# Performance work log

Measured on AMD Instinct MI355X. Metric: run time of the kernel, lower is better.

Reference implementation:

```python
import jax, jax.numpy as jnp
import numpy as np

N_FILTERS = 40
FILTER_SIZE = 401   # int(16000*25/1000), forced odd
POOL_STRIDE = 160   # int(16000*10/1000)
EPS = 1e-6
S_SMOOTH = 0.04     # fixed PCEN smoothing coefficient s
DELTA = 2.0         # fixed PCEN bias delta
R_MIN, R_MAX = 0.2, 1.0
HIDDEN = 32


def setup_inputs() -> dict:
    key = jax.random.key(0)
    ks = jax.random.split(key, 6)
    B, L = 8, 160000
    x = jax.random.normal(ks[0], (B, L), dtype=jnp.float32)
    # mel-initialized Gabor params (as in mel_filter_params)
    sr, fmin, fmax = 16000.0, 60.0, 7800.0
    min_mel = 1127.0 * np.log1p(fmin / 700.0)
    max_mel = 1127.0 * np.log1p(fmax / 700.0)
    peaks_mel = np.linspace(min_mel, max_mel, N_FILTERS + 2)
    peaks_hz = 700.0 * np.expm1(peaks_mel / 1127.0)
    center_freqs = jnp.asarray(peaks_hz[1:-1] * 2.0 * np.pi / sr, dtype=jnp.float32)
    z = np.sqrt(2.0 * np.log(2.0)) / np.pi
    bandwidths = jnp.asarray(z * sr / (peaks_hz[2:] - peaks_hz[:-2]), dtype=jnp.float32)
    pooling_widths = jnp.full((N_FILTERS,), 0.4, dtype=jnp.float32)
    # GRU (input_size=1, hidden=32) + head Linear(32,32)->ReLU->Linear(32,2)
    def gl(k, shape):
        return jax.random.normal(k, shape, dtype=jnp.float32) * 0.1
    w_ih = gl(ks[1], (3 * HIDDEN, 1))
    w_hh = gl(ks[2], (3 * HIDDEN, HIDDEN))
    b_ih = jnp.zeros((3 * HIDDEN,), jnp.float32)
    b_hh = jnp.zeros((3 * HIDDEN,), jnp.float32)
    hw1 = gl(ks[3], (32, HIDDEN)); hb1 = jnp.zeros((32,), jnp.float32)
    hw2 = gl(ks[4], (2, 32)); hb2 = jnp.zeros((2,), jnp.float32)
    return dict(x=x, center_freqs=center_freqs, bandwidths=bandwidths,
                pooling_widths=pooling_widths, w_ih=w_ih, w_hh=w_hh,
                b_ih=b_ih, b_hh=b_hh, hw1=hw1, hb1=hb1, hw2=hw2, hb2=hb2)


def _gabor_filterbank(x, center_freqs, bandwidths, pooling_widths):
    z = np.sqrt(2.0 * np.log(2.0)) / np.pi
    cf = jnp.clip(center_freqs, 0.0, np.pi)
    bw = jnp.clip(bandwidths, 4.0 * z, FILTER_SIZE * z)
    t = jnp.arange(-(FILTER_SIZE // 2), (FILTER_SIZE + 1) // 2, dtype=jnp.float32)
    denom = 1.0 / (jnp.sqrt(2.0 * np.pi) * bw)                        # [F]
    gauss = jnp.exp(-(t[None, :] ** 2) / (2.0 * bw[:, None] ** 2))    # [F,K]
    phase = cf[:, None] * t[None, :]                                  # [F,K]
    fr = denom[:, None] * gauss * jnp.cos(phase)
    fi = denom[:, None] * gauss * jnp.sin(phase)
    filt = jnp.concatenate([fr, fi], axis=0)[:, None, :]              # [2F,1,K]
    pad = FILTER_SIZE // 2
    y = jax.lax.conv_general_dilated(x[:, None, :], filt, (1,), [(pad, pad)])
    y = y ** 2
    y = y[:, :N_FILTERS] + y[:, N_FILTERS:]                           # squared modulus [B,F,L]
    pw = jnp.clip(pooling_widths, 2.0 / FILTER_SIZE, 0.5)
    tt = jnp.arange(FILTER_SIZE, dtype=jnp.float32) / (FILTER_SIZE - 1) - 0.5
    win = jnp.exp(-0.5 * (tt[None, :] / pw[:, None]) ** 2)[:, None, :]  # [F,1,K]
    y = jax.lax.conv_general_dilated(y, win, (POOL_STRIDE,), [(pad, pad)],
                                     feature_group_count=N_FILTERS)
    return y  # [B,F,T]


def _gru_cell(h, xin, w_ih, w_hh, b_ih, b_hh):
    gi = xin @ w_ih.T + b_ih   # [N,3H]
    gh = h @ w_hh.T + b_hh
    i_r, i_z, i_n = jnp.split(gi, 3, axis=-1)
    h_r, h_z, h_n = jnp.split(gh, 3, axis=-1)
    r = jax.nn.sigmoid(i_r + h_r)
    zz = jax.nn.sigmoid(i_z + h_z)
    n = jnp.tanh(i_n + r * h_n)
    return (1.0 - zz) * n + zz * h


def _adaptive_pcen(frames, w_ih, w_hh, b_ih, b_hh, hw1, hb1, hw2, hb2):
    B, F, T = frames.shape
    Xt = jnp.transpose(frames, (2, 0, 1))  # [T,B,F]

    def controller(x_prev, x_t):  # each [B,F] -> per-bin (alpha, r)
        xp = x_prev.reshape(-1, 1)
        xc = x_t.reshape(-1, 1)
        h = jnp.zeros((B * F, HIDDEN), frames.dtype)
        h = _gru_cell(h, xp, w_ih, w_hh, b_ih, b_hh)
        h = _gru_cell(h, xc, w_ih, w_hh, b_ih, b_hh)
        hid = jax.nn.relu(h @ hw1.T + hb1)
        logits = hid @ hw2.T + hb2  # [B*F,2]
        alpha = jax.nn.sigmoid(logits[:, 0]).reshape(B, F)
        r = (R_MIN + (R_MAX - R_MIN) * jax.nn.sigmoid(logits[:, 1])).reshape(B, F)
        return alpha, r

    def step(carry, X_t):
        M_prev, X_prev = carry
        alpha, r = controller(X_prev, X_t)
        M_t = (1.0 - S_SMOOTH) * M_prev + S_SMOOTH * X_t
        out = (X_t / (M_t + EPS) ** alpha + DELTA) ** r - DELTA ** r
        return (M_t, X_t), out

    init = (jnp.zeros((B, F), frames.dtype), Xt[0])
    _, outs = jax.lax.scan(step, init, Xt)
    return jnp.transpose(outs, (1, 2, 0))  # [B,F,T]


def reference(x, center_freqs, bandwidths, pooling_widths,
              w_ih, w_hh, b_ih, b_hh, hw1, hb1, hw2, hb2):
    frames = _gabor_filterbank(x, center_freqs, bandwidths, pooling_widths)
    return _adaptive_pcen(frames, w_ih, w_hh, b_ih, b_hh, hw1, hb1, hw2, hb2)
```

## Files before the change

### kernel.cpp

```cpp
#include <hip/hip_runtime.h>
#include <math.h>

#define NF 40
#define FS 401
#define AST 424
#define PSTRIDE 160
#define BB 8
#define LL 160000
#define PADL 256
#define LST 161024
#define TOUT 1000
#define NTILE 512
#define NCHUNKC 313
#define ROWCH 121
#define ROWST (ROWCH*8)
#define EROW 520
#define WROW 402
#define NCONVB 5032
#define TAUC 125
#define ECH (TAUC*PSTRIDE + 408)

typedef __attribute__((ext_vector_type(8))) _Float16 half8v;
typedef __attribute__((ext_vector_type(4))) _Float16 half4v;
typedef __attribute__((ext_vector_type(2))) _Float16 half2v;
typedef __attribute__((ext_vector_type(4))) float float4v;
typedef _Float16 f16;

__device__ __forceinline__ float sigm(float x) { return 1.0f / (1.0f + __expf(-x)); }
__device__ __forceinline__ float tanh_fast(float x) { return 1.0f - 2.0f / (__expf(2.0f * x) + 1.0f); }

__global__ __launch_bounds__(256) void prep_all(
    const float* __restrict__ x, const float* __restrict__ cf_,
    const float* __restrict__ bw_, const float* __restrict__ pw_,
    f16* __restrict__ xb, f16* __restrict__ Ag, float* __restrict__ winG)
{
    int blk = blockIdx.x;
    if (blk < NCONVB) {
        int i = blk * 256 + threadIdx.x;
        int b = i / LST, o = i % LST;
        float v = 0.0f;
        if (o >= PADL && o < PADL + LL) v = x[b * LL + (o - PADL)];
        xb[i] = (f16)v;
        return;
    }
    const float PI_F = 3.14159265358979323846f;
    if (blk < NCONVB + 80) {
        int row = blk - NCONVB;
        int f = row >> 1, comp = row & 1;
        float Z = sqrtf(2.0f * logf(2.0f)) / PI_F;
        float cf = fminf(fmaxf(cf_[f], 0.0f), PI_F);
        float bw = fminf(fmaxf(bw_[f], 4.0f * Z), 401.0f * Z);
        float denom = 1.0f / (sqrtf(2.0f * PI_F) * bw);
        float inv2 = 1.0f / (2.0f * bw * bw);
        for (int k = threadIdx.x; k < AST; k += 256) {
            float v = 0.0f;
            if (k < FS) {
                float t = (float)(k - 200);
                float g = denom * expf(-(t * t) * inv2);
                float sv, cv;
                sincosf(cf * t, &sv, &cv);
                v = comp ? g * sv : g * cv;
            }
            Ag[row * AST + k] = (f16)v;
        }
        return;
    }
    int f = blk - NCONVB - 80;
    float pw = fminf(fmaxf(pw_[f], 2.0f / 401.0f), 0.5f);
    float invpw = 1.0f / pw;
    for (int j = threadIdx.x; j < WROW; j += 256) {
        float w = 0.0f;
        if (j < FS) {
            float tt = (float)j * (1.0f / 400.0f) - 0.5f;
            float u = tt * invpw;
            w = expf(-0.5f * u * u);
        }
        winG[f * WROW + j] = w;
    }
}

__global__ __launch_bounds__(256, 2) void conv_mfma(
    const f16* __restrict__ xb,
    const f16* __restrict__ Ag,
    f16* __restrict__ eb)
{
    __shared__ __align__(16) unsigned char smem[40 * EROW * 2];
    f16* slab = (f16*)smem;
    f16* eL   = (f16*)smem;

    int chunk = blockIdx.x;
    int bi = blockIdx.y;
    int p0 = chunk * NTILE;
    int pbase = PADL + p0 - 200;
    const f16* xs = xb + (size_t)bi * LST;
    int tid = threadIdx.x;

    for (int sc = tid; sc < 8 * 120; sc += 256) {
        int r = sc / 120, m = sc - r * 120;
        int s0 = pbase + 8 * m + (r & ~1);
        const uint* gp = (const uint*)(xs + s0);
        uint v0 = gp[0], v1 = gp[1], v2 = gp[2], v3 = gp[3], v4 = gp[4];
        if (r & 1) {
            v0 = __builtin_amdgcn_alignbyte(v1, v0, 2);
            v1 = __builtin_amdgcn_alignbyte(v2, v1, 2);
            v2 = __builtin_amdgcn_alignbyte(v3, v2, 2);
            v3 = __builtin_amdgcn_alignbyte(v4, v3, 2);
        }
        *(uint4*)(&slab[r * ROWST + 8 * m]) = make_uint4(v0, v1, v2, v3);
    }
    __syncthreads();

    int wv = tid >> 6, lane = tid & 63, q = lane >> 4, l15 = lane & 15;

    float4v acc[5][8];
#pragma unroll
    for (int t = 0; t < 5; ++t)
#pragma unroll
        for (int s = 0; s < 8; ++s)
            acc[t][s] = (float4v){0.f, 0.f, 0.f, 0.f};

    const f16* aP[5];
    const f16* bPtr[10];
#pragma unroll
    for (int t = 0; t < 5; ++t) aP[t] = Ag + (16 * t + l15) * AST + 8 * q;
#pragma unroll
    for (int s = 0; s < 10; ++s) {
        int pos = 128 * wv + 16 * s + l15;
        bPtr[s] = slab + (pos & 7) * ROWST + 8 * ((pos >> 3) + q);
    }

    half8v bf[8];
#pragma unroll
    for (int s = 0; s < 8; ++s) bf[s] = *(const half8v*)(bPtr[s]);

#pragma unroll
    for (int kk = 0; kk < 13; ++kk) {
        int k = 32 * kk;
        half8v af[5];
#pragma unroll
        for (int t = 0; t < 5; ++t) af[t] = *(const half8v*)(aP[t] + k);
        half8v nb0, nb1;
        if (kk < 12) {
            nb0 = *(const half8v*)(bPtr[8] + k);
            nb1 = *(const half8v*)(bPtr[9] + k);
        }
#pragma unroll
        for (int t = 0; t < 5; ++t)
#pragma unroll
            for (int s = 0; s < 8; ++s)
                acc[t][s] = __builtin_amdgcn_mfma_f32_16x16x32_f16(af[t], bf[s], acc[t][s], 0, 0, 0);
        if (kk < 12) {
#pragma unroll
            for (int s = 0; s < 6; ++s) bf[s] = bf[s + 2];
            bf[6] = nb0; bf[7] = nb1;
        }
    }

    __syncthreads();

#pragma unroll
    for (int t = 0; t < 5; ++t) {
        int f0 = 8 * t + 2 * q;
#pragma unroll
        for (int s = 0; s < 8; ++s) {
            float4v a = acc[t][s];
            int pl = 128 * wv + 16 * s + l15;
            eL[f0 * EROW + pl] = (f16)(a.x * a.x + a.y * a.y);
            eL[(f0 + 1) * EROW + pl] = (f16)(a.z * a.z + a.w * a.w);
        }
    }
    __syncthreads();

    f16* ebb = eb + (size_t)bi * NF * LL;
#pragma unroll
    for (int it = 0; it < 10; ++it) {
        int idx = it * 256 + tid;
        int row = idx >> 6;
        int off = (idx & 63) * 8;
        if (p0 + off < LL) {
            uint4 v = *(const uint4*)(&eL[row * EROW + off]);
            *(uint4*)(&ebb[row * LL + p0 + off]) = v;
        }
    }
}

__global__ __launch_bounds__(1024, 4) void tail_kernel(
    const f16* __restrict__ eb,
    const float* __restrict__ winG,
    const float* __restrict__ w_ih, const float* __restrict__ w_hh,
    const float* __restrict__ b_ih, const float* __restrict__ b_hh,
    const float* __restrict__ hw1, const float* __restrict__ hb1,
    const float* __restrict__ hw2, const float* __restrict__ hb2,
    float* __restrict__ out)
{
    __shared__ __align__(16) float win[416];
    __shared__ __align__(16) float xs[1024];
    __shared__ __align__(16) float ms[1024];
    __shared__ f16 s_whhA[96 * 40];
    __shared__ f16 s_w1A[32 * 40];
    __shared__ __align__(16) float4 s_A1[32];
    __shared__ __align__(16) float4 s_A2[32];
    __shared__ float s_hb1[32];
    __shared__ float s_hw2[64];
    __shared__ float s_hb2[2];
    __shared__ __align__(16) unsigned char ureg[41024];
    f16* es = (f16*)ureg;

    int f = blockIdx.x;
    int bi = blockIdx.y;
    int tid = threadIdx.x;

    for (int i = tid; i < 96 * 32; i += 1024) {
        int m = i >> 5, k = i & 31;
        s_whhA[m * 40 + k] = (f16)w_hh[i];
    }
    for (int i = tid; i < 32 * 32; i += 1024) {
        int m = i >> 5, k = i & 31;
        s_w1A[m * 40 + k] = (f16)hw1[i];
    }
    if (tid < 32) {
        int j = tid;
        s_A1[j] = make_float4(w_ih[j], b_ih[j] + b_hh[j],
                              w_ih[32 + j], b_ih[32 + j] + b_hh[32 + j]);
        s_A2[j] = make_float4(w_ih[64 + j], b_ih[64 + j], b_hh[64 + j], 0.0f);
        s_hb1[j] = hb1[j];
    }
    if (tid < 64) s_hw2[tid] = hw2[tid];
    if (tid < 2)  s_hb2[tid] = hb2[tid];
    if (tid < 416) win[tid] = (tid < WROW) ? winG[f * WROW + tid] : 0.0f;
    if (tid >= 1000) { xs[tid] = 0.0f; ms[tid] = 0.0f; }
    __syncthreads();

    const f16* erow = eb + ((size_t)bi * NF + f) * LL;
    int ft = tid >> 4, l16 = tid & 15;
    for (int c = 0; c < 8; ++c) {
        int start = c * (TAUC * PSTRIDE) - 200;
        if (c > 0 && c < 7) {
            for (int j = tid; j < ECH / 8; j += 1024)
                *(uint4*)(&es[8 * j]) = *(const uint4*)(erow + start + 8 * j);
        } else {
            for (int j = tid; j < ECH; j += 1024) {
                int p = start + j;
                es[j] = (p >= 0 && p < LL) ? erow[p] : (f16)0.0f;
            }
        }
        __syncthreads();
#pragma unroll
        for (int pass = 0; pass < 2; ++pass) {
            int tauL = pass * 64 + ft;
            if (tauL < TAUC) {
                int base = tauL * PSTRIDE;
                float acc = 0.0f;
#pragma unroll
                for (int m = 0; m < 13; ++m) {
                    int kw = 2 * l16 + 32 * m;
                    half2v ep = *(const half2v*)(&es[base + kw]);
                    float2 wp = *(const float2*)(&win[kw]);
                    acc = fmaf((float)ep[0], wp.x, acc);
                    acc = fmaf((float)ep[1], wp.y, acc);
                }
#pragma unroll
                for (int off = 8; off > 0; off >>= 1)
                    acc += __shfl_down(acc, off, 16);
                if (l16 == 0) xs[c * TAUC + tauL] = acc;
            }
        }
        __syncthreads();
    }

    if (tid < 64) {
        int lane = tid;
        const float a1 = 0.96f;
        const float a2 = a1 * a1, a4 = a2 * a2, a8 = a4 * a4;
        const float a16 = a8 * a8, a32 = a16 * a16;
        float al1 = powf(a1, (float)(lane + 1));
        float carry = 0.0f;
        for (int c = 0; c < TOUT; c += 64) {
            float y = 0.04f * xs[c + lane];
            float u;
            u = __shfl_up(y, 1, 64);  if (lane >= 1)  y = fmaf(a1, u, y);
            u = __shfl_up(y, 2, 64);  if (lane >= 2)  y = fmaf(a2, u, y);
            u = __shfl_up(y, 4, 64);  if (lane >= 4)  y = fmaf(a4, u, y);
            u = __shfl_up(y, 8, 64);  if (lane >= 8)  y = fmaf(a8, u, y);
            u = __shfl_up(y, 16, 64); if (lane >= 16) y = fmaf(a16, u, y);
            u = __shfl_up(y, 32, 64); if (lane >= 32) y = fmaf(a32, u, y);
            y = fmaf(al1, carry, y);
            carry = __shfl(y, 63, 64);
            ms[c + lane] = y;
        }
    }
    __syncthreads();

    int wv = tid >> 6, lane = tid & 63;
    int c16 = lane & 15, q = lane >> 4;
    f16* sh1 = (f16*)(ureg + wv * 2560);
    f16* sh2 = (f16*)(ureg + wv * 2560 + 1280);
    float* outb = out + ((size_t)bi * NF + f) * TOUT;

#pragma unroll
    for (int g = 0; g < 4; ++g) {
        int t = (wv * 4 + g) * 16 + c16;
        int tc = (t < TOUT) ? t : (TOUT - 1);
        float xc = xs[tc];
        float xp = (tc == 0) ? xc : xs[tc - 1];
        float mv = ms[tc];

        float h1v[8];
#pragma unroll
        for (int jj = 0; jj < 8; ++jj) {
            int j = (jj < 4) ? (4 * q + jj) : (16 + 4 * q + (jj - 4));
            float4 a1 = s_A1[j];
            float4 a2 = s_A2[j];
            float r = sigm(fmaf(xp, a1.x, a1.y));
            float z = sigm(fmaf(xp, a1.z, a1.w));
            float n = tanh_fast(fmaf(xp, a2.x, a2.y) + r * a2.z);
            h1v[jj] = (1.0f - z) * n;
        }
        {
            half4v lo = {(f16)h1v[0], (f16)h1v[1], (f16)h1v[2], (f16)h1v[3]};
            half4v hi = {(f16)h1v[4], (f16)h1v[5], (f16)h1v[6], (f16)h1v[7]};
            *(half4v*)(&sh1[c16 * 40 + 4 * q]) = lo;
            *(half4v*)(&sh1[c16 * 40 + 16 + 4 * q]) = hi;
        }
        float4v acc[6];
        {
            half8v bfv = *(const half8v*)(&sh1[c16 * 40 + 8 * q]);
#pragma unroll
            for (int tt = 0; tt < 6; ++tt) {
                half8v af = *(const half8v*)(&s_whhA[(16 * tt + c16) * 40 + 8 * q]);
                acc[tt] = __builtin_amdgcn_mfma_f32_16x16x32_f16(af, bfv, (float4v){0.f,0.f,0.f,0.f}, 0, 0, 0);
            }
        }
        float h2v[8];
#pragma unroll
        for (int jj = 0; jj < 8; ++jj) {
            int j = (jj < 4) ? (4 * q + jj) : (16 + 4 * q + (jj - 4));
            int reg = jj & 3;
            float accR = (jj < 4) ? acc[0][reg] : acc[1][reg];
            float accZ = (jj < 4) ? acc[2][reg] : acc[3][reg];
            float accN = (jj < 4) ? acc[4][reg] : acc[5][reg];
            float4 a1 = s_A1[j];
            float4 a2 = s_A2[j];
            float r = sigm(fmaf(xc, a1.x, a1.y) + accR);
            float z = sigm(fmaf(xc, a1.z, a1.w) + accZ);
            float gn = accN + a2.z;
            float n = tanh_fast(fmaf(xc, a2.x, a2.y) + r * gn);
            h2v[jj] = fmaf(z, h1v[jj] - n, n);
        }
        {
            half4v lo = {(f16)h2v[0], (f16)h2v[1], (f16)h2v[2], (f16)h2v[3]};
            half4v hi = {(f16)h2v[4], (f16)h2v[5], (f16)h2v[6], (f16)h2v[7]};
            *(half4v*)(&sh2[c16 * 40 + 4 * q]) = lo;
            *(half4v*)(&sh2[c16 * 40 + 16 + 4 * q]) = hi;
        }
        float4v hacc[2];
        {
            half8v bfv = *(const half8v*)(&sh2[c16 * 40 + 8 * q]);
#pragma unroll
            for (int tt = 0; tt < 2; ++tt) {
                half8v af = *(const half8v*)(&s_w1A[(16 * tt + c16) * 40 + 8 * q]);
                hacc[tt] = __builtin_amdgcn_mfma_f32_16x16x32_f16(af, bfv, (float4v){0.f,0.f,0.f,0.f}, 0, 0, 0);
            }
        }
        float p0 = 0.f, p1 = 0.f;
#pragma unroll
        for (int jj = 0; jj < 8; ++jj) {
            int i = (jj < 4) ? (4 * q + jj) : (16 + 4 * q + (jj - 4));
            int reg = jj & 3;
            float hv = (jj < 4) ? hacc[0][reg] : hacc[1][reg];
            hv = fmaxf(hv + s_hb1[i], 0.0f);
            p0 = fmaf(hv, s_hw2[i], p0);
            p1 = fmaf(hv, s_hw2[32 + i], p1);
        }
        p0 += __shfl_xor(p0, 16);
        p0 += __shfl_xor(p0, 32);
        p1 += __shfl_xor(p1, 16);
        p1 += __shfl_xor(p1, 32);

        float alpha = sigm(p0 + s_hb2[0]);
        float rr = fmaf(0.8f, sigm(p1 + s_hb2[1]), 0.2f);
        float md = __expf(alpha * __logf(mv + 1e-6f));
        float bse = xc / md + 2.0f;
        float val = __expf(rr * __logf(bse)) - __expf(rr * 0.69314718056f);
        if (q == 0 && t < TOUT)
            outb[t] = val;
    }
}

extern "C" void kernel_launch(void* const* d_in, const int* in_sizes, int n_in,
                              void* d_out, int out_size, void* d_ws, size_t ws_size,
                              hipStream_t stream) {
    const float* x    = (const float*)d_in[0];
    const float* cf   = (const float*)d_in[1];
    const float* bw   = (const float*)d_in[2];
    const float* pw   = (const float*)d_in[3];
    const float* w_ih = (const float*)d_in[4];
    const float* w_hh = (const float*)d_in[5];
    const float* b_ih = (const float*)d_in[6];
    const float* b_hh = (const float*)d_in[7];
    const float* hw1  = (const float*)d_in[8];
    const float* hb1  = (const float*)d_in[9];
    const float* hw2  = (const float*)d_in[10];
    const float* hb2  = (const float*)d_in[11];
    float* out = (float*)d_out;

    const size_t xb_b = (size_t)BB * LST * 2;
    const size_t ag_b = (size_t)80 * AST * 2;
    const size_t wg_b = (size_t)NF * WROW * 4;
    size_t fixed = xb_b + ag_b + wg_b;
    size_t e_per_batch = (size_t)NF * LL * 2;
    int nb;
    if (ws_size >= fixed + 8 * e_per_batch)      nb = 8;
    else if (ws_size >= fixed + 2 * e_per_batch) nb = 2;
    else                                         nb = 1;
    int nslice = BB / nb;

    f16* xb     = (f16*)d_ws;
    f16* Ag     = xb + (size_t)BB * LST;
    float* winG = (float*)(Ag + (size_t)80 * AST);
    f16* ebuf   = (f16*)(winG + (size_t)NF * WROW);

    prep_all<<<dim3(NCONVB + 80 + NF), dim3(256), 0, stream>>>(x, cf, bw, pw, xb, Ag, winG);

    for (int sl = 0; sl < nslice; ++sl) {
        conv_mfma<<<dim3(NCHUNKC, nb), dim3(256), 0, stream>>>(
            xb + (size_t)sl * nb * LST, Ag, ebuf);
        tail_kernel<<<dim3(NF, nb), dim3(1024), 0, stream>>>(
            ebuf, winG, w_ih, w_hh, b_ih, b_hh, hw1, hb1, hw2, hb2,
            out + (size_t)sl * nb * NF * TOUT);
    }
}
```

Measured before the change: 299.6 us.

## Fuse fp32-to-fp16 input conversion into conv kernel and shrink tail blocks

Removes the separate padded fp16 copy of the input signal. The conv kernel now reads fp32 samples directly, converts them to half in registers and builds the shifted slab rows with alignbyte, with boundary checks replacing the padding. This drops a full write and re-read of the input and shortens the prep kernel. The tail kernel also moves from 1024 to 512 threads per block, with loops retuned to do more passes per thread, which lowers per-block resources but gives each thread more serial work.

Result: slower. 335.1 us (+11.8%).

```diff
diff --git a/kernel.cpp b/kernel.cpp
--- a/kernel.cpp
+++ b/kernel.cpp
@@ -7,8 +7,6 @@
 #define PSTRIDE 160
 #define BB 8
 #define LL 160000
-#define PADL 256
-#define LST 161024
 #define TOUT 1000
 #define NTILE 512
 #define NCHUNKC 313
@@ -16,7 +14,6 @@
 #define ROWST (ROWCH*8)
 #define EROW 520
 #define WROW 402
-#define NCONVB 5032
 #define TAUC 125
 #define ECH (TAUC*PSTRIDE + 408)
 
@@ -29,23 +26,14 @@
 __device__ __forceinline__ float sigm(float x) { return 1.0f / (1.0f + __expf(-x)); }
 __device__ __forceinline__ float tanh_fast(float x) { return 1.0f - 2.0f / (__expf(2.0f * x) + 1.0f); }
 
-__global__ __launch_bounds__(256) void prep_all(
-    const float* __restrict__ x, const float* __restrict__ cf_,
-    const float* __restrict__ bw_, const float* __restrict__ pw_,
-    f16* __restrict__ xb, f16* __restrict__ Ag, float* __restrict__ winG)
+__global__ __launch_bounds__(256) void prep_small(
+    const float* __restrict__ cf_, const float* __restrict__ bw_,
+    const float* __restrict__ pw_, f16* __restrict__ Ag, float* __restrict__ winG)
 {
+    const float PI_F = 3.14159265358979323846f;
     int blk = blockIdx.x;
-    if (blk < NCONVB) {
-        int i = blk * 256 + threadIdx.x;
-        int b = i / LST, o = i % LST;
-        float v = 0.0f;
-        if (o >= PADL && o < PADL + LL) v = x[b * LL + (o - PADL)];
-        xb[i] = (f16)v;
-        return;
-    }
-    const float PI_F = 3.14159265358979323846f;
-    if (blk < NCONVB + 80) {
-        int row = blk - NCONVB;
+    if (blk < 80) {
+        int row = blk;
         int f = row >> 1, comp = row & 1;
         float Z = sqrtf(2.0f * logf(2.0f)) / PI_F;
         float cf = fminf(fmaxf(cf_[f], 0.0f), PI_F);
@@ -65,7 +53,7 @@
         }
         return;
     }
-    int f = blk - NCONVB - 80;
+    int f = blk - 80;
     float pw = fminf(fmaxf(pw_[f], 2.0f / 401.0f), 0.5f);
     float invpw = 1.0f / pw;
     for (int j = threadIdx.x; j < WROW; j += 256) {
@@ -80,7 +68,7 @@
 }
 
 __global__ __launch_bounds__(256, 2) void conv_mfma(
-    const f16* __restrict__ xb,
+    const float* __restrict__ x,
     const f16* __restrict__ Ag,
     f16* __restrict__ eb)
 {
@@ -91,22 +79,52 @@
     int chunk = blockIdx.x;
     int bi = blockIdx.y;
     int p0 = chunk * NTILE;
-    int pbase = PADL + p0 - 200;
-    const f16* xs = xb + (size_t)bi * LST;
+    int pbase = p0 - 200;
+    const float* xs = x + (size_t)bi * LL;
     int tid = threadIdx.x;
 
-    for (int sc = tid; sc < 8 * 120; sc += 256) {
-        int r = sc / 120, m = sc - r * 120;
-        int s0 = pbase + 8 * m + (r & ~1);
-        const uint* gp = (const uint*)(xs + s0);
-        uint v0 = gp[0], v1 = gp[1], v2 = gp[2], v3 = gp[3], v4 = gp[4];
-        if (r & 1) {
-            v0 = __builtin_amdgcn_alignbyte(v1, v0, 2);
-            v1 = __builtin_amdgcn_alignbyte(v2, v1, 2);
-            v2 = __builtin_amdgcn_alignbyte(v3, v2, 2);
-            v3 = __builtin_amdgcn_alignbyte(v4, v3, 2);
-        }
-        *(uint4*)(&slab[r * ROWST + 8 * m]) = make_uint4(v0, v1, v2, v3);
+    for (int m = tid; m < 120; m += 256) {
+        int g0 = pbase + 8 * m;
+        float fv[16];
+        if (g0 >= 0 && g0 + 16 <= LL) {
+            float4 A = *(const float4*)(xs + g0);
+            float4 Bv = *(const float4*)(xs + g0 + 4);
+            float4 C = *(const float4*)(xs + g0 + 8);
+            float4 D = *(const float4*)(xs + g0 + 12);
+            fv[0]=A.x; fv[1]=A.y; fv[2]=A.z; fv[3]=A.w;
+            fv[4]=Bv.x; fv[5]=Bv.y; fv[6]=Bv.z; fv[7]=Bv.w;
+            fv[8]=C.x; fv[9]=C.y; fv[10]=C.z; fv[11]=C.w;
+            fv[12]=D.x; fv[13]=D.y; fv[14]=D.z; fv[15]=D.w;
+        } else {
+#pragma unroll
+            for (int j = 0; j < 16; ++j) {
+                int gi = g0 + j;
+                fv[j] = (gi >= 0 && gi < LL) ? xs[gi] : 0.0f;
+            }
+        }
+        uint d[8];
+#pragma unroll
+        for (int j = 0; j < 8; ++j) {
+            union { half2v h; uint u; } cv;
+            cv.h[0] = (f16)fv[2 * j];
+            cv.h[1] = (f16)fv[2 * j + 1];
+            d[j] = cv.u;
+        }
+#pragma unroll
+        for (int r = 0; r < 8; r += 2) {
+            int b = r >> 1;
+            *(uint4*)(&slab[r * ROWST + 8 * m]) = make_uint4(d[b], d[b+1], d[b+2], d[b+3]);
+        }
+#pragma unroll
+        for (int r = 1; r < 8; r += 2) {
+            int b = (r - 1) >> 1;
+            uint4 w;
+            w.x = __builtin_amdgcn_alignbyte(d[b+1], d[b],   2);
+            w.y = __builtin_amdgcn_alignbyte(d[b+2], d[b+1], 2);
+            w.z = __builtin_amdgcn_alignbyte(d[b+3], d[b+2], 2);
+            w.w = __builtin_amdgcn_alignbyte(d[b+4], d[b+3], 2);
+            *(uint4*)(&slab[r * ROWST + 8 * m]) = w;
+        }
     }
     __syncthreads();
 
@@ -184,7 +202,7 @@
     }
 }
 
-__global__ __launch_bounds__(1024, 4) void tail_kernel(
+__global__ __launch_bounds__(512, 2) void tail_kernel(
     const f16* __restrict__ eb,
     const float* __restrict__ winG,
     const float* __restrict__ w_ih, const float* __restrict__ w_hh,
@@ -194,8 +212,8 @@
     float* __restrict__ out)
 {
     __shared__ __align__(16) float win[416];
-    __shared__ __align__(16) float xs[1024];
-    __shared__ __align__(16) float ms[1024];
+    __shared__ __align__(16) float xsh[1024];
+    __shared__ __align__(16) float msh[1024];
     __shared__ f16 s_whhA[96 * 40];
     __shared__ f16 s_w1A[32 * 40];
     __shared__ __align__(16) float4 s_A1[32];
@@ -203,18 +221,18 @@
     __shared__ float s_hb1[32];
     __shared__ float s_hw2[64];
     __shared__ float s_hb2[2];
-    __shared__ __align__(16) unsigned char ureg[41024];
+    __shared__ __align__(16) unsigned char ureg[ECH * 2];
     f16* es = (f16*)ureg;
 
     int f = blockIdx.x;
     int bi = blockIdx.y;
     int tid = threadIdx.x;
 
-    for (int i = tid; i < 96 * 32; i += 1024) {
+    for (int i = tid; i < 96 * 32; i += 512) {
         int m = i >> 5, k = i & 31;
         s_whhA[m * 40 + k] = (f16)w_hh[i];
     }
-    for (int i = tid; i < 32 * 32; i += 1024) {
+    for (int i = tid; i < 32 * 32; i += 512) {
         int m = i >> 5, k = i & 31;
         s_w1A[m * 40 + k] = (f16)hw1[i];
     }
@@ -228,7 +246,7 @@
     if (tid < 64) s_hw2[tid] = hw2[tid];
     if (tid < 2)  s_hb2[tid] = hb2[tid];
     if (tid < 416) win[tid] = (tid < WROW) ? winG[f * WROW + tid] : 0.0f;
-    if (tid >= 1000) { xs[tid] = 0.0f; ms[tid] = 0.0f; }
+    if (tid >= 488) { int i = 512 + tid; xsh[i] = 0.0f; msh[i] = 0.0f; }
     __syncthreads();
 
     const f16* erow = eb + ((size_t)bi * NF + f) * LL;
@@ -236,18 +254,18 @@
     for (int c = 0; c < 8; ++c) {
         int start = c * (TAUC * PSTRIDE) - 200;
         if (c > 0 && c < 7) {
-            for (int j = tid; j < ECH / 8; j += 1024)
+            for (int j = tid; j < ECH / 8; j += 512)
                 *(uint4*)(&es[8 * j]) = *(const uint4*)(erow + start + 8 * j);
         } else {
-            for (int j = tid; j < ECH; j += 1024) {
+            for (int j = tid; j < ECH; j += 512) {
                 int p = start + j;
                 es[j] = (p >= 0 && p < LL) ? erow[p] : (f16)0.0f;
             }
         }
         __syncthreads();
 #pragma unroll
-        for (int pass = 0; pass < 2; ++pass) {
-            int tauL = pass * 64 + ft;
+        for (int pass = 0; pass < 4; ++pass) {
+            int tauL = pass * 32 + ft;
             if (tauL < TAUC) {
                 int base = tauL * PSTRIDE;
                 float acc = 0.0f;
@@ -262,7 +280,7 @@
 #pragma unroll
                 for (int off = 8; off > 0; off >>= 1)
                     acc += __shfl_down(acc, off, 16);
-                if (l16 == 0) xs[c * TAUC + tauL] = acc;
+                if (l16 == 0) xsh[c * TAUC + tauL] = acc;
             }
         }
         __syncthreads();
@@ -276,7 +294,7 @@
         float al1 = powf(a1, (float)(lane + 1));
         float carry = 0.0f;
         for (int c = 0; c < TOUT; c += 64) {
-            float y = 0.04f * xs[c + lane];
+            float y = 0.04f * xsh[c + lane];
             float u;
             u = __shfl_up(y, 1, 64);  if (lane >= 1)  y = fmaf(a1, u, y);
             u = __shfl_up(y, 2, 64);  if (lane >= 2)  y = fmaf(a2, u, y);
@@ -286,7 +304,7 @@
             u = __shfl_up(y, 32, 64); if (lane >= 32) y = fmaf(a32, u, y);
             y = fmaf(al1, carry, y);
             carry = __shfl(y, 63, 64);
-            ms[c + lane] = y;
+            msh[c + lane] = y;
         }
     }
     __syncthreads();
@@ -298,12 +316,12 @@
     float* outb = out + ((size_t)bi * NF + f) * TOUT;
 
 #pragma unroll
-    for (int g = 0; g < 4; ++g) {
-        int t = (wv * 4 + g) * 16 + c16;
+    for (int g = 0; g < 8; ++g) {
+        int t = (wv * 8 + g) * 16 + c16;
         int tc = (t < TOUT) ? t : (TOUT - 1);
-        float xc = xs[tc];
-        float xp = (tc == 0) ? xc : xs[tc - 1];
-        float mv = ms[tc];
+        float xc = xsh[tc];
+        float xp = (tc == 0) ? xc : xsh[tc - 1];
+        float mv = msh[tc];
 
         float h1v[8];
 #pragma unroll
@@ -404,10 +422,9 @@
     const float* hb2  = (const float*)d_in[11];
     float* out = (float*)d_out;
 
-    const size_t xb_b = (size_t)BB * LST * 2;
     const size_t ag_b = (size_t)80 * AST * 2;
     const size_t wg_b = (size_t)NF * WROW * 4;
-    size_t fixed = xb_b + ag_b + wg_b;
+    size_t fixed = ag_b + wg_b;
     size_t e_per_batch = (size_t)NF * LL * 2;
     int nb;
     if (ws_size >= fixed + 8 * e_per_batch)      nb = 8;
@@ -415,17 +432,16 @@
     else                                         nb = 1;
     int nslice = BB / nb;
 
-    f16* xb     = (f16*)d_ws;
-    f16* Ag     = xb + (size_t)BB * LST;
+    f16* Ag     = (f16*)d_ws;
     float* winG = (float*)(Ag + (size_t)80 * AST);
     f16* ebuf   = (f16*)(winG + (size_t)NF * WROW);
 
-    prep_all<<<dim3(NCONVB + 80 + NF), dim3(256), 0, stream>>>(x, cf, bw, pw, xb, Ag, winG);
+    prep_small<<<dim3(120), dim3(256), 0, stream>>>(cf, bw, pw, Ag, winG);
 
     for (int sl = 0; sl < nslice; ++sl) {
         conv_mfma<<<dim3(NCHUNKC, nb), dim3(256), 0, stream>>>(
-            xb + (size_t)sl * nb * LST, Ag, ebuf);
-        tail_kernel<<<dim3(NF, nb), dim3(1024), 0, stream>>>(
+            x + (size_t)sl * nb * LL, Ag, ebuf);
+        tail_kernel<<<dim3(NF, nb), dim3(512), 0, stream>>>(
             ebuf, winG, w_ih, w_hh, b_ih, b_hh, hw1, hb1, hw2, hb2,
             out + (size_t)sl * nb * NF * TOUT);
     }
```

## Split tail kernel into parallel pooling kernel and separate scan/controller kernel

Applied to the files above, without the earlier changes.

The fused tail kernel, which ran one 1024-thread block per (batch, filter) and pooled 8 sequential chunks, is split in two. A pool kernel now runs 32 chunks × 40 filters × nb blocks of 256 threads and writes pooled frames to a global buffer. A scan/controller kernel then reads them and does the PCEN scan and the GRU MLP with 256 threads per row. The aim is much more parallelism for the pooling stage, which had only 320 large blocks; the cost is an extra launch and a global round trip for the pooled frames.

Result: faster. 279.3 us (-6.8%).

```diff
diff --git a/kernel.cpp b/kernel.cpp
--- a/kernel.cpp
+++ b/kernel.cpp
@@ -16,9 +16,10 @@
 #define ROWST (ROWCH*8)
 #define EROW 520
 #define WROW 402
+#define TCP 32
+#define NCHUNKP 32
+#define PELEM (TCP*PSTRIDE + 408)
 #define NCONVB 5032
-#define TAUC 125
-#define ECH (TAUC*PSTRIDE + 408)
 
 typedef __attribute__((ext_vector_type(8))) _Float16 half8v;
 typedef __attribute__((ext_vector_type(4))) _Float16 half4v;
@@ -184,18 +185,66 @@
     }
 }
 
-__global__ __launch_bounds__(1024, 4) void tail_kernel(
-    const f16* __restrict__ eb,
-    const float* __restrict__ winG,
+__global__ __launch_bounds__(256) void pool_kernel(
+    const f16* __restrict__ eb, const float* __restrict__ winG, float* __restrict__ Xout)
+{
+    __shared__ __align__(16) f16 es[PELEM + 8];
+    __shared__ __align__(16) float win[416];
+    int chunk = blockIdx.x;
+    int f = blockIdx.y;
+    int bi = blockIdx.z;
+    int tau0 = chunk * TCP;
+    int start = tau0 * PSTRIDE - 200;
+    int tid = threadIdx.x;
+
+    for (int k = tid; k < 416; k += 256)
+        win[k] = (k < WROW) ? winG[f * WROW + k] : 0.0f;
+
+    const f16* erow = eb + ((size_t)bi * NF + f) * LL;
+    if (start >= 0 && start + PELEM <= LL) {
+        for (int j = tid; j < PELEM / 8; j += 256)
+            *(uint4*)(&es[8 * j]) = *(const uint4*)(erow + start + 8 * j);
+    } else {
+        for (int j = tid; j < PELEM; j += 256) {
+            int p = start + j;
+            es[j] = (p >= 0 && p < LL) ? erow[p] : (f16)0.0f;
+        }
+    }
+    __syncthreads();
+
+    int ft = tid >> 4, l16 = tid & 15;
+#pragma unroll
+    for (int pass = 0; pass < 2; ++pass) {
+        int frame = pass * 16 + ft;
+        int base = frame * PSTRIDE;
+        float acc = 0.0f;
+#pragma unroll
+        for (int m = 0; m < 13; ++m) {
+            int kw = 2 * l16 + 32 * m;
+            half2v ep = *(const half2v*)(&es[base + kw]);
+            float2 wp = *(const float2*)(&win[kw]);
+            acc = fmaf((float)ep[0], wp.x, acc);
+            acc = fmaf((float)ep[1], wp.y, acc);
+        }
+#pragma unroll
+        for (int off = 8; off > 0; off >>= 1)
+            acc += __shfl_down(acc, off, 16);
+        int tau = tau0 + frame;
+        if (l16 == 0 && tau < TOUT)
+            Xout[((size_t)bi * NF + f) * TOUT + tau] = acc;
+    }
+}
+
+__global__ __launch_bounds__(256) void scanctrl_kernel(
+    const float* __restrict__ X,
     const float* __restrict__ w_ih, const float* __restrict__ w_hh,
     const float* __restrict__ b_ih, const float* __restrict__ b_hh,
     const float* __restrict__ hw1, const float* __restrict__ hb1,
     const float* __restrict__ hw2, const float* __restrict__ hb2,
     float* __restrict__ out)
 {
-    __shared__ __align__(16) float win[416];
-    __shared__ __align__(16) float xs[1024];
-    __shared__ __align__(16) float ms[1024];
+    __shared__ __align__(16) float xsh[1024];
+    __shared__ __align__(16) float msh[1024];
     __shared__ f16 s_whhA[96 * 40];
     __shared__ f16 s_w1A[32 * 40];
     __shared__ __align__(16) float4 s_A1[32];
@@ -203,18 +252,18 @@
     __shared__ float s_hb1[32];
     __shared__ float s_hw2[64];
     __shared__ float s_hb2[2];
-    __shared__ __align__(16) unsigned char ureg[41024];
-    f16* es = (f16*)ureg;
-
-    int f = blockIdx.x;
-    int bi = blockIdx.y;
+    __shared__ f16 sh1[4][16 * 40];
+    __shared__ f16 sh2[4][16 * 40];
+
+    int bin = blockIdx.x;
     int tid = threadIdx.x;
-
-    for (int i = tid; i < 96 * 32; i += 1024) {
+    const float* Xrow = X + (size_t)bin * TOUT;
+
+    for (int i = tid; i < 96 * 32; i += 256) {
         int m = i >> 5, k = i & 31;
         s_whhA[m * 40 + k] = (f16)w_hh[i];
     }
-    for (int i = tid; i < 32 * 32; i += 1024) {
+    for (int i = tid; i < 32 * 32; i += 256) {
         int m = i >> 5, k = i & 31;
         s_w1A[m * 40 + k] = (f16)hw1[i];
     }
@@ -227,46 +276,9 @@
     }
     if (tid < 64) s_hw2[tid] = hw2[tid];
     if (tid < 2)  s_hb2[tid] = hb2[tid];
-    if (tid < 416) win[tid] = (tid < WROW) ? winG[f * WROW + tid] : 0.0f;
-    if (tid >= 1000) { xs[tid] = 0.0f; ms[tid] = 0.0f; }
-    __syncthreads();
-
-    const f16* erow = eb + ((size_t)bi * NF + f) * LL;
-    int ft = tid >> 4, l16 = tid & 15;
-    for (int c = 0; c < 8; ++c) {
-        int start = c * (TAUC * PSTRIDE) - 200;
-        if (c > 0 && c < 7) {
-            for (int j = tid; j < ECH / 8; j += 1024)
-                *(uint4*)(&es[8 * j]) = *(const uint4*)(erow + start + 8 * j);
-        } else {
-            for (int j = tid; j < ECH; j += 1024) {
-                int p = start + j;
-                es[j] = (p >= 0 && p < LL) ? erow[p] : (f16)0.0f;
-            }
-        }
-        __syncthreads();
-#pragma unroll
-        for (int pass = 0; pass < 2; ++pass) {
-            int tauL = pass * 64 + ft;
-            if (tauL < TAUC) {
-                int base = tauL * PSTRIDE;
-                float acc = 0.0f;
-#pragma unroll
-                for (int m = 0; m < 13; ++m) {
-                    int kw = 2 * l16 + 32 * m;
-                    half2v ep = *(const half2v*)(&es[base + kw]);
-                    float2 wp = *(const float2*)(&win[kw]);
-                    acc = fmaf((float)ep[0], wp.x, acc);
-                    acc = fmaf((float)ep[1], wp.y, acc);
-                }
-#pragma unroll
-                for (int off = 8; off > 0; off >>= 1)
-                    acc += __shfl_down(acc, off, 16);
-                if (l16 == 0) xs[c * TAUC + tauL] = acc;
-            }
-        }
-        __syncthreads();
-    }
+    for (int i = tid; i < 1024; i += 256)
+        xsh[i] = (i < TOUT) ? Xrow[i] : 0.0f;
+    __syncthreads();
 
     if (tid < 64) {
         int lane = tid;
@@ -276,7 +288,7 @@
         float al1 = powf(a1, (float)(lane + 1));
         float carry = 0.0f;
         for (int c = 0; c < TOUT; c += 64) {
-            float y = 0.04f * xs[c + lane];
+            float y = 0.04f * xsh[c + lane];
             float u;
             u = __shfl_up(y, 1, 64);  if (lane >= 1)  y = fmaf(a1, u, y);
             u = __shfl_up(y, 2, 64);  if (lane >= 2)  y = fmaf(a2, u, y);
@@ -286,24 +298,22 @@
             u = __shfl_up(y, 32, 64); if (lane >= 32) y = fmaf(a32, u, y);
             y = fmaf(al1, carry, y);
             carry = __shfl(y, 63, 64);
-            ms[c + lane] = y;
+            msh[c + lane] = y;
         }
     }
     __syncthreads();
 
     int wv = tid >> 6, lane = tid & 63;
     int c16 = lane & 15, q = lane >> 4;
-    f16* sh1 = (f16*)(ureg + wv * 2560);
-    f16* sh2 = (f16*)(ureg + wv * 2560 + 1280);
-    float* outb = out + ((size_t)bi * NF + f) * TOUT;
-
-#pragma unroll
-    for (int g = 0; g < 4; ++g) {
-        int t = (wv * 4 + g) * 16 + c16;
+    float* outb = out + (size_t)bin * TOUT;
+
+#pragma unroll 2
+    for (int g = 0; g < 16; ++g) {
+        int t = (wv * 16 + g) * 16 + c16;
         int tc = (t < TOUT) ? t : (TOUT - 1);
-        float xc = xs[tc];
-        float xp = (tc == 0) ? xc : xs[tc - 1];
-        float mv = ms[tc];
+        float xc = xsh[tc];
+        float xp = (tc == 0) ? xc : xsh[tc - 1];
+        float mv = msh[tc];
 
         float h1v[8];
 #pragma unroll
@@ -319,12 +329,12 @@
         {
             half4v lo = {(f16)h1v[0], (f16)h1v[1], (f16)h1v[2], (f16)h1v[3]};
             half4v hi = {(f16)h1v[4], (f16)h1v[5], (f16)h1v[6], (f16)h1v[7]};
-            *(half4v*)(&sh1[c16 * 40 + 4 * q]) = lo;
-            *(half4v*)(&sh1[c16 * 40 + 16 + 4 * q]) = hi;
+            *(half4v*)(&sh1[wv][c16 * 40 + 4 * q]) = lo;
+            *(half4v*)(&sh1[wv][c16 * 40 + 16 + 4 * q]) = hi;
         }
         float4v acc[6];
         {
-            half8v bfv = *(const half8v*)(&sh1[c16 * 40 + 8 * q]);
+            half8v bfv = *(const half8v*)(&sh1[wv][c16 * 40 + 8 * q]);
 #pragma unroll
             for (int tt = 0; tt < 6; ++tt) {
                 half8v af = *(const half8v*)(&s_whhA[(16 * tt + c16) * 40 + 8 * q]);
@@ -350,12 +360,12 @@
         {
             half4v lo = {(f16)h2v[0], (f16)h2v[1], (f16)h2v[2], (f16)h2v[3]};
             half4v hi = {(f16)h2v[4], (f16)h2v[5], (f16)h2v[6], (f16)h2v[7]};
-            *(half4v*)(&sh2[c16 * 40 + 4 * q]) = lo;
-            *(half4v*)(&sh2[c16 * 40 + 16 + 4 * q]) = hi;
+            *(half4v*)(&sh2[wv][c16 * 40 + 4 * q]) = lo;
+            *(half4v*)(&sh2[wv][c16 * 40 + 16 + 4 * q]) = hi;
         }
         float4v hacc[2];
         {
-            half8v bfv = *(const half8v*)(&sh2[c16 * 40 + 8 * q]);
+            half8v bfv = *(const half8v*)(&sh2[wv][c16 * 40 + 8 * q]);
 #pragma unroll
             for (int tt = 0; tt < 2; ++tt) {
                 half8v af = *(const half8v*)(&s_w1A[(16 * tt + c16) * 40 + 8 * q]);
@@ -408,7 +418,7 @@
     const size_t ag_b = (size_t)80 * AST * 2;
     const size_t wg_b = (size_t)NF * WROW * 4;
     size_t fixed = xb_b + ag_b + wg_b;
-    size_t e_per_batch = (size_t)NF * LL * 2;
+    size_t e_per_batch = (size_t)NF * LL * 2 + (size_t)NF * TOUT * 4;
     int nb;
     if (ws_size >= fixed + 8 * e_per_batch)      nb = 8;
     else if (ws_size >= fixed + 2 * e_per_batch) nb = 2;
@@ -419,14 +429,17 @@
     f16* Ag     = xb + (size_t)BB * LST;
     float* winG = (float*)(Ag + (size_t)80 * AST);
     f16* ebuf   = (f16*)(winG + (size_t)NF * WROW);
+    float* Xf   = (float*)(ebuf + (size_t)nb * NF * LL);
 
     prep_all<<<dim3(NCONVB + 80 + NF), dim3(256), 0, stream>>>(x, cf, bw, pw, xb, Ag, winG);
 
     for (int sl = 0; sl < nslice; ++sl) {
         conv_mfma<<<dim3(NCHUNKC, nb), dim3(256), 0, stream>>>(
             xb + (size_t)sl * nb * LST, Ag, ebuf);
-        tail_kernel<<<dim3(NF, nb), dim3(1024), 0, stream>>>(
-            ebuf, winG, w_ih, w_hh, b_ih, b_hh, hw1, hb1, hw2, hb2,
+        pool_kernel<<<dim3(NCHUNKP, NF, nb), dim3(256), 0, stream>>>(
+            ebuf, winG, Xf);
+        scanctrl_kernel<<<dim3(nb * NF), dim3(256), 0, stream>>>(
+            Xf, w_ih, w_hh, b_ih, b_hh, hw1, hb1, hw2, hb2,
             out + (size_t)sl * nb * NF * TOUT);
     }
 }
```
